# Kernel tuning notes

Measured on AMD Instinct MI355X. Metric: run time of the kernel, lower is better.

## Reference

```python
import jax, jax.numpy as jnp
import numpy as np

B, E, H, SEQ = 4096, 512, 512, 128


def setup_inputs() -> dict:
    key = jax.random.key(0)
    ks = jax.random.split(key, 7)
    s = 1.0 / np.sqrt(H)  # PyTorch LSTM init scale
    return {
        "start_emb": jax.random.normal(ks[0], (B, 1, E), dtype=jnp.float32),
        "h0": jax.random.normal(ks[1], (1, B, H), dtype=jnp.float32),
        "c0": jax.random.normal(ks[2], (1, B, H), dtype=jnp.float32),
        "w_ih": jax.random.normal(ks[3], (4 * H, E), dtype=jnp.float32) * s,
        "w_hh": jax.random.normal(ks[4], (4 * H, H), dtype=jnp.float32) * s,
        "b_ih": jax.random.normal(ks[5], (4 * H,), dtype=jnp.float32) * s,
        "b_hh": jax.random.normal(ks[6], (4 * H,), dtype=jnp.float32) * s,
        "seq_length": SEQ,
    }


def reference(start_emb, h0, c0, w_ih, w_hh, b_ih, b_hh, seq_length):
    # start_emb: [B, 1, E] -- identical input every step, so precompute its projection once.
    x = start_emb[:, 0, :]                       # [B, E]
    x_proj = x @ w_ih.T + b_ih + b_hh            # [B, 4H], constant across steps
    hdim = w_hh.shape[1]

    def step(carry, _):
        h, c = carry                              # each [B, H]
        gates = x_proj + h @ w_hh.T               # [B, 4H]
        i, f, g, o = jnp.split(gates, 4, axis=-1) # PyTorch gate order i,f,g,o
        i = jax.nn.sigmoid(i)
        f = jax.nn.sigmoid(f)
        g = jnp.tanh(g)
        o = jax.nn.sigmoid(o)
        c = f * c + i * g
        h = o * jnp.tanh(c)
        return (h, c), None

    (h, c), _ = jax.lax.scan(step, (h0[0], c0[0]), None, length=seq_length)
    # Return final (h_n, c_n) with the [num_layers=1, B, H] leading dim, as PyTorch does.
    return h[None], c[None]
```

## Files before the change

kernel.cpp:

```cpp
#include <hip/hip_runtime.h>
#include <hip/hip_bf16.h>

#define BATCH 4096
#define KD    512
#define NG    2048
#define SEQLEN 128

typedef __attribute__((ext_vector_type(8))) short short8;
typedef __attribute__((ext_vector_type(4))) float floatx4;

#define HWREG_XCC_ID (20 | (0 << 6) | ((4 - 1) << 11))

__device__ __forceinline__ void gld16(const void* g, void* l) {
  __builtin_amdgcn_global_load_lds(
      (const __attribute__((address_space(1))) void*)g,
      (__attribute__((address_space(3))) void*)l, 16, 0, 0);
}

__device__ __forceinline__ float fast_sig(float x) {
  return __builtin_amdgcn_rcpf(1.0f + __expf(-x));
}
__device__ __forceinline__ float fast_tanh(float x) {
  return 1.0f - 2.0f * __builtin_amdgcn_rcpf(1.0f + __expf(2.0f * x));
}

__device__ __forceinline__ unsigned pack_bf16(float lo, float hi) {
  unsigned ul = (unsigned)__builtin_bit_cast(unsigned short, __float2bfloat16(lo));
  unsigned uh = (unsigned)__builtin_bit_cast(unsigned short, __float2bfloat16(hi));
  return (uh << 16) | ul;
}
__device__ __forceinline__ float unpack_lo(unsigned u) {
  u <<= 16; return __builtin_bit_cast(float, u);
}
__device__ __forceinline__ float unpack_hi(unsigned u) {
  u &= 0xffff0000u; return __builtin_bit_cast(float, u);
}

__device__ __forceinline__ void load_panel128(const short* __restrict__ W, int bn,
                                              short* __restrict__ lWB, int tid) {
#pragma unroll
  for (int i = 0; i < 16; ++i) {
    int q = i * 512 + tid;
    int kt = q >> 10;
    int rem = q & 1023;
    int row = rem >> 3, cc = rem & 7;
    int cs = cc ^ (row & 7);
    gld16(W + (size_t)(bn + row) * KD + (kt * 8 + cs) * 8, lWB + q * 8);
  }
}

__device__ __forceinline__ void stageA32(const short* __restrict__ A, int bm,
                                         int p, short* __restrict__ dst, int tid) {
  const int k0 = p * 32;
#pragma unroll
  for (int i = 0; i < 2; ++i) {
    int q = i * 512 + tid;
    int lr = q >> 3, c1 = q & 7;
    int c0 = c1 ^ (lr & 7);
    int row = lr * 2 + (c0 >> 2);
    int kc = c0 & 3;
    gld16(A + (size_t)(bm + row) * KD + k0 + kc * 8, dst + q * 8);
  }
}

__device__ __forceinline__ void compute32(const short* __restrict__ lWB,
                                          const short* __restrict__ lA,
                                          floatx4 acc[4][4], int p,
                                          int lane, int wm, int wn) {
  short8 a[4], b[4];
  const int kt = p >> 1;
  const int kb = (p & 1) * 4 + (lane >> 4);
#pragma unroll
  for (int j = 0; j < 4; ++j) {
    int brow = wn * 64 + j * 16 + (lane & 15);
    int cc = kb ^ (brow & 7);
    b[j] = *(const short8*)&lWB[kt * 8192 + brow * 64 + cc * 8];
  }
#pragma unroll
  for (int mi = 0; mi < 4; ++mi) {
    int arow = wm * 64 + mi * 16 + (lane & 15);
    int lr = arow >> 1;
    int cc = (((arow & 1) << 2) + (lane >> 4)) ^ (lr & 7);
    a[mi] = *(const short8*)&lA[lr * 64 + cc * 8];
  }
#pragma unroll
  for (int mi = 0; mi < 4; ++mi)
#pragma unroll
    for (int j = 0; j < 4; ++j)
      acc[mi][j] =
          __builtin_amdgcn_mfma_f32_16x16x32_bf16(a[mi], b[j], acc[mi][j], 0, 0, 0);
}

__device__ __forceinline__ void gemm_dbuf(const short* __restrict__ A,
                                          const short* __restrict__ lWB,
                                          short* __restrict__ lAb,
                                          floatx4 acc[4][4],
                                          int bm, int lane, int wm, int wn,
                                          int tid) {
  stageA32(A, bm, 0, lAb, tid);
  __syncthreads();
#pragma unroll 2
  for (int p = 0; p < 16; ++p) {
    if (p < 15) stageA32(A, bm, p + 1, lAb + ((p + 1) & 1) * 8192, tid);
    compute32(lWB, lAb + (p & 1) * 8192, acc, p, lane, wm, wn);
    __syncthreads();
  }
}

template <int TBM, int TBN, int NT>
__device__ __forceinline__ void gemm_tile(const short* __restrict__ A,
                                          const short* __restrict__ Bw,
                                          floatx4 acc[4][4],
                                          short* lA, short* lB,
                                          int bm, int bn,
                                          int lane, int wm, int wn, int tid) {
#pragma unroll 1
  for (int kt = 0; kt < KD / 64; ++kt) {
    const int k0 = kt * 64;
#pragma unroll
    for (int i = 0; i < TBM * 8 / NT; ++i) {
      int q = i * NT + tid;
      int row = q >> 3, cs = q & 7;
      int cc = cs ^ (row & 7);
      gld16(A + (size_t)(bm + row) * KD + k0 + cc * 8, lA + q * 8);
    }
#pragma unroll
    for (int i = 0; i < TBN * 8 / NT; ++i) {
      int q = i * NT + tid;
      int row = q >> 3, cs = q & 7;
      int cc = cs ^ (row & 7);
      gld16(Bw + (size_t)(bn + row) * KD + k0 + cc * 8, lB + q * 8);
    }
    __syncthreads();
#pragma unroll
    for (int ks = 0; ks < 2; ++ks) {
      short8 a[4], b[4];
#pragma unroll
      for (int mi = 0; mi < 4; ++mi) {
        int arow = wm * 64 + mi * 16 + (lane & 15);
        int ch = (ks * 4 + (lane >> 4)) ^ (arow & 7);
        a[mi] = *(const short8*)&lA[arow * 64 + ch * 8];
      }
#pragma unroll
      for (int j = 0; j < 4; ++j) {
        int brow = wn * 64 + j * 16 + (lane & 15);
        int ch = (ks * 4 + (lane >> 4)) ^ (brow & 7);
        b[j] = *(const short8*)&lB[brow * 64 + ch * 8];
      }
#pragma unroll
      for (int mi = 0; mi < 4; ++mi)
#pragma unroll
        for (int j = 0; j < 4; ++j)
          acc[mi][j] =
              __builtin_amdgcn_mfma_f32_16x16x32_bf16(a[mi], b[j], acc[mi][j], 0, 0, 0);
    }
    __syncthreads();
  }
}

__device__ __forceinline__ void group_barrier_xcd(unsigned* cnt, unsigned target) {
  __syncthreads();
  if (threadIdx.x == 0) {
    __hip_atomic_fetch_add(cnt, 1u, __ATOMIC_RELAXED, __HIP_MEMORY_SCOPE_AGENT);
    unsigned guard = 0;
    while (__hip_atomic_load(cnt, __ATOMIC_RELAXED, __HIP_MEMORY_SCOPE_AGENT) <
               target &&
           ++guard < (1u << 20)) {
      __builtin_amdgcn_s_sleep(1);
    }
    asm volatile("buffer_inv sc0" ::: "memory");
    asm volatile("s_waitcnt vmcnt(0)" ::: "memory");
  }
  __syncthreads();
}

__global__ __launch_bounds__(512, 1) void lstm_persist(
    const short* __restrict__ xbf,
    const short* __restrict__ wih,
    const short* __restrict__ whh,
    const float* __restrict__ biasp,
    const float* __restrict__ c0,
    short* __restrict__ hA, short* __restrict__ hB,
    float* __restrict__ outH, float* __restrict__ outC,
    unsigned* __restrict__ sync_area) {
  extern __shared__ __align__(16) char dsm[];
  short* lWB = (short*)dsm;
  short* lAb = (short*)(dsm + 131072);

  const int tid = threadIdx.x;
  const int lane = tid & 63;
  const int wid = tid >> 6;
  const int wm = wid >> 1;
  const int wn = wid & 1;

  if (tid == 0) {
    int px = __builtin_amdgcn_s_getreg(HWREG_XCC_ID) & 7;
    unsigned r = __hip_atomic_fetch_add(&sync_area[px], 1u, __ATOMIC_RELAXED,
                                        __HIP_MEMORY_SCOPE_AGENT);
    ((int*)lAb)[0] = px * 2 + (int)((r >> 4) & 1);
    ((int*)lAb)[1] = (int)(r & 15);
  }
  __syncthreads();
  const int gid = ((int*)lAb)[0];
  const int by  = ((int*)lAb)[1];
  __syncthreads();
  const int bm = gid * 256;
  const int bn = by * 128;
  unsigned* gcnt = sync_area + 256 + gid * 32;

  const int houter = by * 2 + wn;
  const int hcol = houter * 16 + (lane & 15);
  const int rb = houter * 64 + (lane & 15);

  load_panel128(wih, bn, lWB, tid);
  __syncthreads();
  floatx4 acc[4][4] = {};
  gemm_dbuf(xbf, lWB, lAb, acc, bm, lane, wm, wn, tid);

  const float b0 = biasp[rb], b1 = biasp[rb + 16], b2 = biasp[rb + 32],
              b3 = biasp[rb + 48];
  unsigned xprP[4][4][2];
  float creg[4][4];
#pragma unroll
  for (int mi = 0; mi < 4; ++mi) {
    const int mrow0 = bm + wm * 64 + mi * 16 + (lane >> 4) * 4;
#pragma unroll
    for (int reg = 0; reg < 4; ++reg) {
      xprP[mi][reg][0] = pack_bf16(acc[mi][0][reg] + b0, acc[mi][1][reg] + b1);
      xprP[mi][reg][1] = pack_bf16(acc[mi][2][reg] + b2, acc[mi][3][reg] + b3);
      creg[mi][reg] = c0[(size_t)(mrow0 + reg) * KD + hcol];
    }
  }

  load_panel128(whh, bn, lWB, tid);
  __syncthreads();

#pragma unroll 1
  for (int t = 0; t < SEQLEN; ++t) {
    const short* hin = (t & 1) ? hB : hA;
    short* hout = (t & 1) ? hA : hB;

#pragma unroll
    for (int mi = 0; mi < 4; ++mi)
#pragma unroll
      for (int j = 0; j < 4; ++j)
        acc[mi][j] = floatx4{0.f, 0.f, 0.f, 0.f};

    gemm_dbuf(hin, lWB, lAb, acc, bm, lane, wm, wn, tid);

#pragma unroll
    for (int mi = 0; mi < 4; ++mi) {
      const int mrow0 = bm + wm * 64 + mi * 16 + (lane >> 4) * 4;
#pragma unroll
      for (int reg = 0; reg < 4; ++reg) {
        const int m = mrow0 + reg;
        float gi = acc[mi][0][reg] + unpack_lo(xprP[mi][reg][0]);
        float gf = acc[mi][1][reg] + unpack_hi(xprP[mi][reg][0]);
        float gg = acc[mi][2][reg] + unpack_lo(xprP[mi][reg][1]);
        float go = acc[mi][3][reg] + unpack_hi(xprP[mi][reg][1]);
        float si = fast_sig(gi);
        float sf = fast_sig(gf);
        float tg = fast_tanh(gg);
        float so = fast_sig(go);
        float cn = sf * creg[mi][reg] + si * tg;
        creg[mi][reg] = cn;
        float hn = so * fast_tanh(cn);
        const size_t ci = (size_t)m * KD + hcol;
        ((__hip_bfloat16*)hout)[ci] = __float2bfloat16(hn);
        if (t == SEQLEN - 1) {
          outH[ci] = hn;
          outC[ci] = cn;
        }
      }
    }
    if (t != SEQLEN - 1) group_barrier_xcd(gcnt, 16u * (unsigned)(t + 1));
  }
}

__global__ __launch_bounds__(256, 2) void lstm_step(
    const short* __restrict__ hin, __hip_bfloat16* __restrict__ hout_bf,
    const short* __restrict__ W, const float* __restrict__ xp,
    float* __restrict__ c, float* __restrict__ hout_f32) {
  __shared__ __align__(16) short lA[128 * 64];
  __shared__ __align__(16) short lB[128 * 64];
  const int tid = threadIdx.x;
  const int lane = tid & 63;
  const int wid = tid >> 6;
  const int wm = wid >> 1, wn = wid & 1;
  const int bm = blockIdx.x * 128, bn = blockIdx.y * 128;

  floatx4 acc[4][4] = {};
  gemm_tile<128, 128, 256>(hin, W, acc, lA, lB, bm, bn, lane, wm, wn, tid);

  const int houter = blockIdx.y * 2 + wn;
  const int hcol = houter * 16 + (lane & 15);
  const int rb = houter * 64 + (lane & 15);
#pragma unroll
  for (int mi = 0; mi < 4; ++mi) {
    const int mrow0 = bm + wm * 64 + mi * 16 + (lane >> 4) * 4;
#pragma unroll
    for (int reg = 0; reg < 4; ++reg) {
      const int m = mrow0 + reg;
      const float* xpr = xp + (size_t)m * NG + rb;
      float si = fast_sig(acc[mi][0][reg] + xpr[0]);
      float sf = fast_sig(acc[mi][1][reg] + xpr[16]);
      float tg = fast_tanh(acc[mi][2][reg] + xpr[32]);
      float so = fast_sig(acc[mi][3][reg] + xpr[48]);
      const int ci = m * KD + hcol;
      float cn = sf * c[ci] + si * tg;
      c[ci] = cn;
      float hn = so * fast_tanh(cn);
      hout_bf[ci] = __float2bfloat16(hn);
      if (hout_f32) hout_f32[ci] = hn;
    }
  }
}

__global__ __launch_bounds__(256, 2) void xproj_gemm(
    const short* __restrict__ xbf, const short* __restrict__ Wih,
    const float* __restrict__ biasp, float* __restrict__ xp) {
  __shared__ __align__(16) short lA[128 * 64];
  __shared__ __align__(16) short lB[128 * 64];
  const int tid = threadIdx.x;
  const int lane = tid & 63;
  const int wid = tid >> 6;
  const int wm = wid >> 1, wn = wid & 1;
  const int bm = blockIdx.x * 128, bn = blockIdx.y * 128;

  floatx4 acc[4][4] = {};
  gemm_tile<128, 128, 256>(xbf, Wih, acc, lA, lB, bm, bn, lane, wm, wn, tid);

  const int houter = blockIdx.y * 2 + wn;
  const int rb = houter * 64 + (lane & 15);
  const float b0 = biasp[rb], b1 = biasp[rb + 16], b2 = biasp[rb + 32],
              b3 = biasp[rb + 48];
#pragma unroll
  for (int mi = 0; mi < 4; ++mi) {
    const int mrow0 = bm + wm * 64 + mi * 16 + (lane >> 4) * 4;
#pragma unroll
    for (int reg = 0; reg < 4; ++reg) {
      float* xpr = xp + (size_t)(mrow0 + reg) * NG + rb;
      xpr[0]  = acc[mi][0][reg] + b0;
      xpr[16] = acc[mi][1][reg] + b1;
      xpr[32] = acc[mi][2][reg] + b2;
      xpr[48] = acc[mi][3][reg] + b3;
    }
  }
}

__global__ void permw_k(const float* __restrict__ w,
                        __hip_bfloat16* __restrict__ o) {
  int idx = blockIdx.x * 256 + threadIdx.x;
  int r = idx >> 9, k = idx & 511;
  int hout = r >> 6, g = (r >> 4) & 3, hin = r & 15;
  o[idx] = __float2bfloat16(w[(size_t)((g << 9) + hout * 16 + hin) * 512 + k]);
}

__global__ void bias_k(const float* __restrict__ bi, const float* __restrict__ bh,
                       float* __restrict__ o) {
  int r = blockIdx.x * 256 + threadIdx.x;
  int hout = r >> 6, g = (r >> 4) & 3, hin = r & 15;
  int n = (g << 9) + hout * 16 + hin;
  o[r] = bi[n] + bh[n];
}

__global__ void f2bf_k(const float* __restrict__ in,
                       __hip_bfloat16* __restrict__ out, int n) {
  int i = blockIdx.x * 256 + threadIdx.x;
  if (i < n) out[i] = __float2bfloat16(in[i]);
}

extern "C" void kernel_launch(void* const* d_in, const int* in_sizes, int n_in,
                              void* d_out, int out_size, void* d_ws, size_t ws_size,
                              hipStream_t stream) {
  const float* start_emb = (const float*)d_in[0];
  const float* h0 = (const float*)d_in[1];
  const float* c0 = (const float*)d_in[2];
  const float* w_ih = (const float*)d_in[3];
  const float* w_hh = (const float*)d_in[4];
  const float* b_ih = (const float*)d_in[5];
  const float* b_hh = (const float*)d_in[6];

  char* ws = (char*)d_ws;
  __hip_bfloat16* whh_p = (__hip_bfloat16*)(ws);
  __hip_bfloat16* wih_p = (__hip_bfloat16*)(ws + (2ll << 20));
  __hip_bfloat16* xbf   = (__hip_bfloat16*)(ws + (4ll << 20));
  __hip_bfloat16* hbufA = (__hip_bfloat16*)(ws + (8ll << 20));
  __hip_bfloat16* hbufB = (__hip_bfloat16*)(ws + (12ll << 20));
  float* biasp          = (float*)(ws + (16ll << 20));
  unsigned* sync_area   = (unsigned*)(ws + (16ll << 20) + 65536);
  float* xp             = (float*)(ws + (17ll << 20));

  float* outH = (float*)d_out;
  float* outC = (float*)d_out + (size_t)BATCH * KD;

  permw_k<<<4096, 256, 0, stream>>>(w_hh, whh_p);
  permw_k<<<4096, 256, 0, stream>>>(w_ih, wih_p);
  bias_k<<<8, 256, 0, stream>>>(b_ih, b_hh, biasp);
  f2bf_k<<<8192, 256, 0, stream>>>(start_emb, xbf, BATCH * KD);
  f2bf_k<<<8192, 256, 0, stream>>>(h0, hbufA, BATCH * KD);
  (void)hipMemsetAsync(sync_area, 0, 8192, stream);

  const short* a_xbf = (const short*)xbf;
  const short* a_wih = (const short*)wih_p;
  const short* a_whh = (const short*)whh_p;
  const float* a_bias = biasp;
  const float* a_c0 = c0;
  short* a_hA = (short*)hbufA;
  short* a_hB = (short*)hbufB;
  float* a_outH = outH;
  float* a_outC = outC;
  unsigned* a_sync = sync_area;
  void* args[] = {&a_xbf, &a_wih, &a_whh, &a_bias, &a_c0,
                  &a_hA, &a_hB, &a_outH, &a_outC, &a_sync};
  hipError_t e = hipLaunchCooperativeKernel((const void*)lstm_persist,
                                            dim3(256), dim3(512), args,
                                            163840, stream);
  if (e != hipSuccess) {
    (void)hipMemcpyAsync(outC, c0, (size_t)BATCH * KD * sizeof(float),
                         hipMemcpyDeviceToDevice, stream);
    dim3 grid(BATCH / 128, NG / 128);
    xproj_gemm<<<grid, 256, 0, stream>>>((const short*)xbf, (const short*)wih_p,
                                         biasp, xp);
    for (int t = 0; t < SEQLEN; ++t) {
      const short* hin = (const short*)((t & 1) ? hbufB : hbufA);
      __hip_bfloat16* hout = (t & 1) ? hbufA : hbufB;
      lstm_step<<<grid, 256, 0, stream>>>(hin, hout, (const short*)whh_p, xp,
                                          outC, (t == SEQLEN - 1) ? outH : nullptr);
    }
  }
}
```

Measured before the change: 1.445 ms.

## Triple-buffer A staging and keep last weight K-slab in registers

The LDS weight panel shrinks from eight to seven K-slabs, and the last slab's B fragments are held in per-wave registers. The freed LDS holds a third A staging buffer, so the h-tile loads now run two stages ahead. The per-stage __syncthreads becomes a partial vmcnt wait plus a raw s_barrier, so more global loads can be in flight while the MFMAs run. The cost is higher register pressure from the eight extra short8 values, and the hand-written waitcnt and barrier sequence must stay correct with respect to buffer reuse.

After: 1.786 ms. +23.6%, slower.

```diff
diff --git a/kernel.cpp b/kernel.cpp
--- a/kernel.cpp
+++ b/kernel.cpp
@@ -36,10 +36,10 @@
   u &= 0xffff0000u; return __builtin_bit_cast(float, u);
 }
 
-__device__ __forceinline__ void load_panel128(const short* __restrict__ W, int bn,
+__device__ __forceinline__ void load_panel112(const short* __restrict__ W, int bn,
                                               short* __restrict__ lWB, int tid) {
 #pragma unroll
-  for (int i = 0; i < 16; ++i) {
+  for (int i = 0; i < 14; ++i) {
     int q = i * 512 + tid;
     int kt = q >> 10;
     int rem = q & 1023;
@@ -47,6 +47,18 @@
     int cs = cc ^ (row & 7);
     gld16(W + (size_t)(bn + row) * KD + (kt * 8 + cs) * 8, lWB + q * 8);
   }
+}
+
+__device__ __forceinline__ void load_b7(const short* __restrict__ W, int bn,
+                                        int wn, int lane, short8 b7[8]) {
+#pragma unroll
+  for (int h = 0; h < 2; ++h)
+#pragma unroll
+    for (int j = 0; j < 4; ++j) {
+      int brow = wn * 64 + j * 16 + (lane & 15);
+      b7[h * 4 + j] = *(const short8*)
+          &W[(size_t)(bn + brow) * KD + (size_t)(56 + h * 4 + (lane >> 4)) * 8];
+    }
 }
 
 __device__ __forceinline__ void stageA32(const short* __restrict__ A, int bm,
@@ -63,48 +75,59 @@
   }
 }
 
-__device__ __forceinline__ void compute32(const short* __restrict__ lWB,
-                                          const short* __restrict__ lA,
-                                          floatx4 acc[4][4], int p,
-                                          int lane, int wm, int wn) {
-  short8 a[4], b[4];
-  const int kt = p >> 1;
-  const int kb = (p & 1) * 4 + (lane >> 4);
-#pragma unroll
-  for (int j = 0; j < 4; ++j) {
-    int brow = wn * 64 + j * 16 + (lane & 15);
-    int cc = kb ^ (brow & 7);
-    b[j] = *(const short8*)&lWB[kt * 8192 + brow * 64 + cc * 8];
-  }
-#pragma unroll
-  for (int mi = 0; mi < 4; ++mi) {
-    int arow = wm * 64 + mi * 16 + (lane & 15);
-    int lr = arow >> 1;
-    int cc = (((arow & 1) << 2) + (lane >> 4)) ^ (lr & 7);
-    a[mi] = *(const short8*)&lA[lr * 64 + cc * 8];
-  }
-#pragma unroll
-  for (int mi = 0; mi < 4; ++mi)
-#pragma unroll
-    for (int j = 0; j < 4; ++j)
-      acc[mi][j] =
-          __builtin_amdgcn_mfma_f32_16x16x32_bf16(a[mi], b[j], acc[mi][j], 0, 0, 0);
-}
-
-__device__ __forceinline__ void gemm_dbuf(const short* __restrict__ A,
+__device__ __forceinline__ void gemm_pipe(const short* __restrict__ A,
                                           const short* __restrict__ lWB,
                                           short* __restrict__ lAb,
+                                          const short8 b7reg[8],
                                           floatx4 acc[4][4],
                                           int bm, int lane, int wm, int wn,
                                           int tid) {
   stageA32(A, bm, 0, lAb, tid);
-  __syncthreads();
-#pragma unroll 2
+  stageA32(A, bm, 1, lAb + 8192, tid);
+  asm volatile("s_waitcnt vmcnt(2)" ::: "memory");
+  __builtin_amdgcn_sched_barrier(0);
+  __builtin_amdgcn_s_barrier();
+#pragma unroll
   for (int p = 0; p < 16; ++p) {
-    if (p < 15) stageA32(A, bm, p + 1, lAb + ((p + 1) & 1) * 8192, tid);
-    compute32(lWB, lAb + (p & 1) * 8192, acc, p, lane, wm, wn);
-    __syncthreads();
-  }
+    if (p < 14) stageA32(A, bm, p + 2, lAb + ((p + 2) % 3) * 8192, tid);
+    const short* lA = lAb + (p % 3) * 8192;
+    short8 a[4], b[4];
+    const int kb = (p & 1) * 4 + (lane >> 4);
+    if (p < 14) {
+      const int kt = p >> 1;
+#pragma unroll
+      for (int j = 0; j < 4; ++j) {
+        int brow = wn * 64 + j * 16 + (lane & 15);
+        int cc = kb ^ (brow & 7);
+        b[j] = *(const short8*)&lWB[kt * 8192 + brow * 64 + cc * 8];
+      }
+    } else {
+#pragma unroll
+      for (int j = 0; j < 4; ++j) b[j] = b7reg[(p & 1) * 4 + j];
+    }
+#pragma unroll
+    for (int mi = 0; mi < 4; ++mi) {
+      int arow = wm * 64 + mi * 16 + (lane & 15);
+      int lr = arow >> 1;
+      int cc = (((arow & 1) << 2) + (lane >> 4)) ^ (lr & 7);
+      a[mi] = *(const short8*)&lA[lr * 64 + cc * 8];
+    }
+#pragma unroll
+    for (int mi = 0; mi < 4; ++mi)
+#pragma unroll
+      for (int j = 0; j < 4; ++j)
+        acc[mi][j] =
+            __builtin_amdgcn_mfma_f32_16x16x32_bf16(a[mi], b[j], acc[mi][j], 0, 0, 0);
+    if (p < 15) {
+      if (p == 14)
+        asm volatile("s_waitcnt vmcnt(0) lgkmcnt(0)" ::: "memory");
+      else
+        asm volatile("s_waitcnt vmcnt(2) lgkmcnt(0)" ::: "memory");
+      __builtin_amdgcn_sched_barrier(0);
+      __builtin_amdgcn_s_barrier();
+    }
+  }
+  __syncthreads();
 }
 
 template <int TBM, int TBN, int NT>
@@ -185,7 +208,7 @@
     unsigned* __restrict__ sync_area) {
   extern __shared__ __align__(16) char dsm[];
   short* lWB = (short*)dsm;
-  short* lAb = (short*)(dsm + 131072);
+  short* lAb = (short*)(dsm + 114688);
 
   const int tid = threadIdx.x;
   const int lane = tid & 63;
@@ -212,10 +235,13 @@
   const int hcol = houter * 16 + (lane & 15);
   const int rb = houter * 64 + (lane & 15);
 
-  load_panel128(wih, bn, lWB, tid);
+  short8 b7reg[8];
+
+  load_panel112(wih, bn, lWB, tid);
+  load_b7(wih, bn, wn, lane, b7reg);
   __syncthreads();
   floatx4 acc[4][4] = {};
-  gemm_dbuf(xbf, lWB, lAb, acc, bm, lane, wm, wn, tid);
+  gemm_pipe(xbf, lWB, lAb, b7reg, acc, bm, lane, wm, wn, tid);
 
   const float b0 = biasp[rb], b1 = biasp[rb + 16], b2 = biasp[rb + 32],
               b3 = biasp[rb + 48];
@@ -232,7 +258,8 @@
     }
   }
 
-  load_panel128(whh, bn, lWB, tid);
+  load_b7(whh, bn, wn, lane, b7reg);
+  load_panel112(whh, bn, lWB, tid);
   __syncthreads();
 
 #pragma unroll 1
@@ -246,7 +273,7 @@
       for (int j = 0; j < 4; ++j)
         acc[mi][j] = floatx4{0.f, 0.f, 0.f, 0.f};
 
-    gemm_dbuf(hin, lWB, lAb, acc, bm, lane, wm, wn, tid);
+    gemm_pipe(hin, lWB, lAb, b7reg, acc, bm, lane, wm, wn, tid);
 
 #pragma unroll
     for (int mi = 0; mi < 4; ++mi) {
```

## Replace per-step group barrier with per-producer flags waited per K-chunk

Applied to the files above, without the earlier changes.

Replaces the all-blocks group barrier at the end of each timestep with one progress flag per producer block. A consumer waits only for the producer of the next K-chunk of h before staging it, so the recurrent GEMM can start on chunks that are already ready. The h loads now use a cache-bypassing aux bit instead of an explicit buffer invalidate. The intent is to remove barrier stalls and let blocks within a group drift. The cost is relaxed flag stores with no release fence, which could expose stale h data, and a larger sync area to clear.

New measurement: 1.840 ms. 1.27x slower.

```diff
diff --git a/kernel.cpp b/kernel.cpp
--- a/kernel.cpp
+++ b/kernel.cpp
@@ -11,10 +11,11 @@
 
 #define HWREG_XCC_ID (20 | (0 << 6) | ((4 - 1) << 11))
 
+template <int AUX>
 __device__ __forceinline__ void gld16(const void* g, void* l) {
   __builtin_amdgcn_global_load_lds(
       (const __attribute__((address_space(1))) void*)g,
-      (__attribute__((address_space(3))) void*)l, 16, 0, 0);
+      (__attribute__((address_space(3))) void*)l, 16, 0, AUX);
 }
 
 __device__ __forceinline__ float fast_sig(float x) {
@@ -34,6 +35,14 @@
 }
 __device__ __forceinline__ float unpack_hi(unsigned u) {
   u &= 0xffff0000u; return __builtin_bit_cast(float, u);
+}
+
+__device__ __forceinline__ void wait_flag(const unsigned* f, unsigned want) {
+  unsigned guard = 0;
+  while (__hip_atomic_load(f, __ATOMIC_RELAXED, __HIP_MEMORY_SCOPE_AGENT) < want &&
+         ++guard < (1u << 20)) {
+    __builtin_amdgcn_s_sleep(1);
+  }
 }
 
 __device__ __forceinline__ void load_panel128(const short* __restrict__ W, int bn,
@@ -45,7 +54,7 @@
     int rem = q & 1023;
     int row = rem >> 3, cc = rem & 7;
     int cs = cc ^ (row & 7);
-    gld16(W + (size_t)(bn + row) * KD + (kt * 8 + cs) * 8, lWB + q * 8);
+    gld16<0>(W + (size_t)(bn + row) * KD + (kt * 8 + cs) * 8, lWB + q * 8);
   }
 }
 
@@ -59,7 +68,7 @@
     int c0 = c1 ^ (lr & 7);
     int row = lr * 2 + (c0 >> 2);
     int kc = c0 & 3;
-    gld16(A + (size_t)(bm + row) * KD + k0 + kc * 8, dst + q * 8);
+    gld16<1>(A + (size_t)(bm + row) * KD + k0 + kc * 8, dst + q * 8);
   }
 }
 
@@ -96,13 +105,21 @@
                                           short* __restrict__ lAb,
                                           floatx4 acc[4][4],
                                           int bm, int lane, int wm, int wn,
-                                          int tid) {
+                                          int tid, const unsigned* flags,
+                                          unsigned want) {
+  if (flags != nullptr && tid == 0) {
+    wait_flag(flags + 0 * 32, want);
+    wait_flag(flags + 1 * 32, want);
+  }
+  __syncthreads();
   stageA32(A, bm, 0, lAb, tid);
   __syncthreads();
 #pragma unroll 2
   for (int p = 0; p < 16; ++p) {
     if (p < 15) stageA32(A, bm, p + 1, lAb + ((p + 1) & 1) * 8192, tid);
     compute32(lWB, lAb + (p & 1) * 8192, acc, p, lane, wm, wn);
+    if (flags != nullptr && p < 14 && tid == 0)
+      wait_flag(flags + (p + 2) * 32, want);
     __syncthreads();
   }
 }
@@ -122,14 +139,14 @@
       int q = i * NT + tid;
       int row = q >> 3, cs = q & 7;
       int cc = cs ^ (row & 7);
-      gld16(A + (size_t)(bm + row) * KD + k0 + cc * 8, lA + q * 8);
+      gld16<0>(A + (size_t)(bm + row) * KD + k0 + cc * 8, lA + q * 8);
     }
 #pragma unroll
     for (int i = 0; i < TBN * 8 / NT; ++i) {
       int q = i * NT + tid;
       int row = q >> 3, cs = q & 7;
       int cc = cs ^ (row & 7);
-      gld16(Bw + (size_t)(bn + row) * KD + k0 + cc * 8, lB + q * 8);
+      gld16<0>(Bw + (size_t)(bn + row) * KD + k0 + cc * 8, lB + q * 8);
     }
     __syncthreads();
 #pragma unroll
@@ -156,22 +173,6 @@
     }
     __syncthreads();
   }
-}
-
-__device__ __forceinline__ void group_barrier_xcd(unsigned* cnt, unsigned target) {
-  __syncthreads();
-  if (threadIdx.x == 0) {
-    __hip_atomic_fetch_add(cnt, 1u, __ATOMIC_RELAXED, __HIP_MEMORY_SCOPE_AGENT);
-    unsigned guard = 0;
-    while (__hip_atomic_load(cnt, __ATOMIC_RELAXED, __HIP_MEMORY_SCOPE_AGENT) <
-               target &&
-           ++guard < (1u << 20)) {
-      __builtin_amdgcn_s_sleep(1);
-    }
-    asm volatile("buffer_inv sc0" ::: "memory");
-    asm volatile("s_waitcnt vmcnt(0)" ::: "memory");
-  }
-  __syncthreads();
 }
 
 __global__ __launch_bounds__(512, 1) void lstm_persist(
@@ -206,7 +207,8 @@
   __syncthreads();
   const int bm = gid * 256;
   const int bn = by * 128;
-  unsigned* gcnt = sync_area + 256 + gid * 32;
+  unsigned* flags = sync_area + 512 + gid * 512;
+  unsigned* myflag = flags + by * 32;
 
   const int houter = by * 2 + wn;
   const int hcol = houter * 16 + (lane & 15);
@@ -215,7 +217,7 @@
   load_panel128(wih, bn, lWB, tid);
   __syncthreads();
   floatx4 acc[4][4] = {};
-  gemm_dbuf(xbf, lWB, lAb, acc, bm, lane, wm, wn, tid);
+  gemm_dbuf(xbf, lWB, lAb, acc, bm, lane, wm, wn, tid, nullptr, 0u);
 
   const float b0 = biasp[rb], b1 = biasp[rb + 16], b2 = biasp[rb + 32],
               b3 = biasp[rb + 48];
@@ -246,7 +248,7 @@
       for (int j = 0; j < 4; ++j)
         acc[mi][j] = floatx4{0.f, 0.f, 0.f, 0.f};
 
-    gemm_dbuf(hin, lWB, lAb, acc, bm, lane, wm, wn, tid);
+    gemm_dbuf(hin, lWB, lAb, acc, bm, lane, wm, wn, tid, flags, (unsigned)t);
 
 #pragma unroll
     for (int mi = 0; mi < 4; ++mi) {
@@ -273,7 +275,12 @@
         }
       }
     }
-    if (t != SEQLEN - 1) group_barrier_xcd(gcnt, 16u * (unsigned)(t + 1));
+    if (t != SEQLEN - 1) {
+      __syncthreads();
+      if (tid == 0)
+        __hip_atomic_store(myflag, (unsigned)(t + 1), __ATOMIC_RELAXED,
+                           __HIP_MEMORY_SCOPE_AGENT);
+    }
   }
 }
 
@@ -399,7 +406,7 @@
   bias_k<<<8, 256, 0, stream>>>(b_ih, b_hh, biasp);
   f2bf_k<<<8192, 256, 0, stream>>>(start_emb, xbf, BATCH * KD);
   f2bf_k<<<8192, 256, 0, stream>>>(h0, hbufA, BATCH * KD);
-  (void)hipMemsetAsync(sync_area, 0, 8192, stream);
+  (void)hipMemsetAsync(sync_area, 0, 36864, stream);
 
   const short* a_xbf = (const short*)xbf;
   const short* a_wih = (const short*)wih_p;
```
